# Kernel tuning notes

Hardware: AMD Instinct MI355X
Metric: run time of the kernel (lower is better)

## Reference

```python
import jax, jax.numpy as jnp
import numpy as np

B = 32          # graphs per batch
NPG = 2048      # nodes per graph
N = B * NPG     # 65536 total nodes
EPG = 16384     # edges per graph
E = B * EPG     # 524288 total edges
F_IN = 129
H, C = 4, 64    # heads, per-head channels
HC = H * C      # 256
NEG_SLOPE = 0.2 # GATConv LeakyReLU slope


def setup_inputs() -> dict:
    key = jax.random.key(0)
    ks = jax.random.split(key, 20)
    # node features
    x = jax.random.normal(ks[0], (N, F_IN), dtype=jnp.float32)
    # random edges, endpoints within the same graph (per-graph contiguous node ids)
    off = (jnp.arange(B) * NPG)[:, None]
    src = (jax.random.randint(ks[1], (B, EPG), 0, NPG) + off).reshape(-1)
    dst = (jax.random.randint(ks[2], (B, EPG), 0, NPG) + off).reshape(-1)
    edge_index = jnp.stack([src, dst]).astype(jnp.int64)

    def lin(k, fan_in, shape):
        return jax.random.normal(k, shape, dtype=jnp.float32) / np.sqrt(fan_in)

    return {
        "x": x,
        "edge_index": edge_index,
        "lin0_w": lin(ks[3], F_IN, (F_IN, 256)),
        "lin0_b": jnp.zeros((256,), jnp.float32),
        "gat0_W": lin(ks[4], 256, (256, HC)),
        "gat0_asrc": lin(ks[5], C, (H, C)),
        "gat0_adst": lin(ks[6], C, (H, C)),
        "gat0_b": jnp.zeros((HC,), jnp.float32),
        "pool0_w": lin(ks[7], HC, (HC,)),
        "gat1_W": lin(ks[8], HC, (HC, HC)),
        "gat1_asrc": lin(ks[9], C, (H, C)),
        "gat1_adst": lin(ks[10], C, (H, C)),
        "gat1_b": jnp.zeros((HC,), jnp.float32),
        "pool1_w": lin(ks[11], HC, (HC,)),
        "gate_w": lin(ks[12], HC, (HC, 1)),
        "gate_b": jnp.zeros((1,), jnp.float32),
    }


def _leaky(z):
    return jnp.where(z > 0, z, NEG_SLOPE * z)


def _gat(h_in, src, dst, emask, W, asrc, adst, b):
    """PyG GATConv: shared lin, edge attention, segment softmax over dest, self-loops, concat heads."""
    n = h_in.shape[0]
    h = (h_in @ W).reshape(n, H, C)                       # [n,H,C]
    loops = jnp.arange(n)
    s = jnp.concatenate([src, loops])                     # add self loops
    d = jnp.concatenate([dst, loops])
    m = jnp.concatenate([emask, jnp.ones((n,), bool)])
    a_s = jnp.einsum('nhc,hc->nh', h, asrc)               # [n,H]
    a_d = jnp.einsum('nhc,hc->nh', h, adst)
    logit = _leaky(a_s[s] + a_d[d])                       # [E+n,H]
    logit = jnp.where(m[:, None], logit, -1e9)
    mx = jax.ops.segment_max(logit, d, num_segments=n)    # stable segment softmax
    ex = jnp.exp(logit - mx[d]) * m[:, None].astype(logit.dtype)
    den = jax.ops.segment_sum(ex, d, num_segments=n)
    coef = ex / (den[d] + 1e-16)                          # [E+n,H]
    out = jax.ops.segment_sum(h[s] * coef[:, :, None], d, num_segments=n)
    return out.reshape(n, HC) + b


def _topk_pool(hx, src, dst, emask, w, n_in, k):
    """PyG TopKPooling: score = x.w/||w||, per-graph top-k, x' = x[perm]*tanh(score[perm]), edge filter+reindex."""
    n_tot = hx.shape[0]
    bb = n_tot // n_in
    score = (hx @ w) / (jnp.linalg.norm(w) + 1e-16)       # [n_tot]
    _, idx = jax.lax.top_k(score.reshape(bb, n_in), k)    # [bb,k]
    perm = (idx + (jnp.arange(bb) * n_in)[:, None]).reshape(-1)
    xs = hx[perm] * jnp.tanh(score[perm])[:, None]
    newid = jnp.full((n_tot,), -1, jnp.int32).at[perm].set(jnp.arange(bb * k, dtype=jnp.int32))
    ns, nd = newid[src], newid[dst]
    valid = emask & (ns >= 0) & (nd >= 0)
    ns = jnp.where(valid, ns, 0)
    nd = jnp.where(valid, nd, 0)
    return xs, ns, nd, valid


def _attpool(hx, n, gate_w, gate_b):
    """AttentionalAggregation: softmax(gate_nn(x)) per graph, weighted sum."""
    bb = hx.shape[0] // n
    gate = (hx @ gate_w + gate_b).reshape(bb, n)
    wts = jax.nn.softmax(gate, axis=1)
    return jnp.einsum('bn,bnf->bf', wts, hx.reshape(bb, n, -1))


def reference(x, edge_index, lin0_w, lin0_b, gat0_W, gat0_asrc, gat0_adst, gat0_b,
              pool0_w, gat1_W, gat1_asrc, gat1_adst, gat1_b, pool1_w, gate_w, gate_b):
    src, dst = edge_index[0], edge_index[1]
    emask = jnp.ones((E,), bool)
    h = jax.nn.relu(x @ lin0_w + lin0_b)                                  # hidden MLP
    h = jax.nn.elu(_gat(h, src, dst, emask, gat0_W, gat0_asrc, gat0_adst, gat0_b))
    h, src, dst, emask = _topk_pool(h, src, dst, emask, pool0_w, NPG, NPG // 2)
    out = _attpool(h, NPG // 2, gate_w, gate_b)                           # [B,256]
    h = jax.nn.elu(_gat(h, src, dst, emask, gat1_W, gat1_asrc, gat1_adst, gat1_b))
    h, src, dst, emask = _topk_pool(h, src, dst, emask, pool1_w, NPG // 2, NPG // 4)
    out = out + _attpool(h, NPG // 4, gate_w, gate_b)
    return out
```

## Files before the change

### kernel.cpp

```cpp
#include <hip/hip_runtime.h>
#include <cmath>

namespace {

constexpr int NN0 = 65536;
constexpr int NB  = 32;
constexpr int NE  = 524288;
constexpr int FIN = 129;
constexpr int KP  = 160;

typedef short bf16x8 __attribute__((ext_vector_type(8)));
typedef float f32x4 __attribute__((ext_vector_type(4)));

__device__ inline float leakyrelu(float z) { return z > 0.f ? z : 0.2f * z; }
__device__ inline float eluf(float z) { return z > 0.f ? z : expm1f(z); }

__device__ inline unsigned short f2bf(float x) {
  union { float f; unsigned int u; } v; v.f = x;
  unsigned int r = v.u + 0x7fffu + ((v.u >> 16) & 1u);
  return (unsigned short)(r >> 16);
}
__device__ inline float bf2f(unsigned short h) {
  union { unsigned int u; float f; } v; v.u = ((unsigned int)h) << 16;
  return v.f;
}

__device__ inline float4 f4fma(float4 a, float c, float4 acc) {
  acc.x += a.x * c; acc.y += a.y * c; acc.z += a.z * c; acc.w += a.w * c;
  return acc;
}

__device__ inline int swz_block(int bid, int bpgl) {
  int x = bid & 7;
  int local = bid >> 3;
  int g = x + ((local >> bpgl) << 3);
  return (g << bpgl) + (local & ((1 << bpgl) - 1));
}

__device__ __forceinline__ void gload_lds16(const unsigned short* g, unsigned short* l) {
  __builtin_amdgcn_global_load_lds((const unsigned int*)g, (unsigned int*)l, 16, 0, 0);
}

__device__ inline void pack_w_body(const float* __restrict__ W, int Kreal, int idx,
                                   unsigned short* __restrict__ hi,
                                   unsigned short* __restrict__ lo) {
  int j = idx & 7;
  int lane = (idx >> 3) & 63;
  int ct = (idx >> 9) & 15;
  int kt = idx >> 13;
  int k = kt * 32 + ((lane >> 4) << 3) + j;
  int c = ct * 16 + (lane & 15);
  float v = (k < Kreal) ? W[(size_t)k * 256 + c] : 0.f;
  unsigned short h = f2bf(v);
  hi[idx] = h;
  lo[idx] = f2bf(v - bf2f(h));
}

__global__ void prep(const float* __restrict__ x,
                     const float* __restrict__ w0, const float* __restrict__ w1,
                     const float* __restrict__ w2,
                     const float* __restrict__ pw0, const float* __restrict__ pw1,
                     unsigned short* __restrict__ xhi, unsigned short* __restrict__ xlo,
                     unsigned short* __restrict__ whi0, unsigned short* __restrict__ wlo0,
                     unsigned short* __restrict__ whi1, unsigned short* __restrict__ wlo1,
                     unsigned short* __restrict__ whi2, unsigned short* __restrict__ wlo2,
                     float* __restrict__ norms, int* __restrict__ cursor,
                     int* __restrict__ cursor2, int* __restrict__ newid) {
  const int NX = NN0 * KP / 256;
  const int NW0 = 5 * 8192 / 256;
  const int NW = 8 * 8192 / 256;
  const int NC = NN0 / 256;
  int b = blockIdx.x, tid = threadIdx.x;
  if (b < NX) {
    int idx = b * 256 + tid;
    int row = idx / KP, c = idx - row * KP;
    float v = (c < FIN) ? x[(size_t)row * FIN + c] : 0.f;
    unsigned short h = f2bf(v);
    xhi[idx] = h;
    xlo[idx] = f2bf(v - bf2f(h));
    return;
  }
  b -= NX;
  if (b < NW0) { pack_w_body(w0, FIN, b * 256 + tid, whi0, wlo0); return; }
  b -= NW0;
  if (b < NW) { pack_w_body(w1, 256, b * 256 + tid, whi1, wlo1); return; }
  b -= NW;
  if (b < NW) { pack_w_body(w2, 256, b * 256 + tid, whi2, wlo2); return; }
  b -= NW;
  if (b < NC) {
    int i = b * 256 + tid;
    cursor[i] = 0;
    newid[i] = -1;
    if (i < 32768) cursor2[i] = 0;
    return;
  }
  if (tid < 64) {
    float a0 = 0.f, a1 = 0.f;
#pragma unroll
    for (int j = tid; j < 256; j += 64) {
      float v0 = pw0[j]; a0 += v0 * v0;
      float v1 = pw1[j]; a1 += v1 * v1;
    }
#pragma unroll
    for (int off = 32; off >= 1; off >>= 1) {
      a0 += __shfl_xor(a0, off);
      a1 += __shfl_xor(a1, off);
    }
    if (tid == 0) {
      norms[0] = 1.f / (sqrtf(a0) + 1e-16f);
      norms[1] = 1.f / (sqrtf(a1) + 1e-16f);
    }
  }
}

template <int KT, bool RELUBIAS, bool ATT, bool INDIR>
__global__ __launch_bounds__(256, 2) void gemm_mfma(
    const unsigned short* __restrict__ Xhi, const unsigned short* __restrict__ Xlo,
    int ldx,
    const unsigned short* __restrict__ Bhi, const unsigned short* __restrict__ Blo,
    const float* __restrict__ bias,
    float* __restrict__ Out,
    unsigned short* __restrict__ OutHi, unsigned short* __restrict__ OutLo,
    const float* __restrict__ attsrc, const float* __restrict__ attdst,
    float* __restrict__ a_s, float* __restrict__ a_d,
    const int* __restrict__ rowmap, const float* __restrict__ tscale, int swzl) {
  __shared__ __align__(16) unsigned short As[2][2][128][32];
  const int tid = threadIdx.x;
  const int lane = tid & 63;
  const int w = tid >> 6;
  const int rb = (swzl >= 0) ? swz_block(blockIdx.x, swzl) : blockIdx.x;
  const int row0 = rb * 128;
  const int l15 = lane & 15, q = lane >> 4;
  const int sl4 = lane >> 2;
  const int skc = (lane & 3) * 8;

  size_t gr[2];
#pragma unroll
  for (int i = 0; i < 2; i++) {
    int lr = row0 + (w + 4 * i) * 16 + sl4;
    gr[i] = INDIR ? (size_t)rowmap[lr] : (size_t)lr;
  }

  auto stage = [&](int nb, int kt) {
#pragma unroll
    for (int i = 0; i < 2; i++) {
      const int rbase = (w + 4 * i) * 16;
      const size_t goff = gr[i] * ldx + kt * 32 + skc;
      gload_lds16(Xhi + goff, &As[nb][0][rbase][0]);
      gload_lds16(Xlo + goff, &As[nb][1][rbase][0]);
    }
  };

  f32x4 acc[8][4];
#pragma unroll
  for (int mf = 0; mf < 8; mf++)
#pragma unroll
    for (int nf = 0; nf < 4; nf++) acc[mf][nf] = (f32x4)(0.f);

  stage(0, 0);
  __syncthreads();

#pragma unroll
  for (int kt = 0; kt < KT; ++kt) {
    const int nb = kt & 1;
    if (kt + 1 < KT) stage(nb ^ 1, kt + 1);
    bf16x8 bh[4], bl[4];
#pragma unroll
    for (int nf = 0; nf < 4; nf++) {
      const int ct = w * 4 + nf;
      const size_t bbase = ((size_t)((kt * 16 + ct) * 64 + lane)) << 3;
      bh[nf] = *reinterpret_cast<const bf16x8*>(Bhi + bbase);
      bl[nf] = *reinterpret_cast<const bf16x8*>(Blo + bbase);
    }
#pragma unroll
    for (int mf = 0; mf < 8; mf++) {
      const int ar = mf * 16 + l15;
      bf16x8 ah = *reinterpret_cast<const bf16x8*>(&As[nb][0][ar][q * 8]);
      bf16x8 al = *reinterpret_cast<const bf16x8*>(&As[nb][1][ar][q * 8]);
#pragma unroll
      for (int nf = 0; nf < 4; nf++) {
        acc[mf][nf] = __builtin_amdgcn_mfma_f32_16x16x32_bf16(ah, bh[nf], acc[mf][nf], 0, 0, 0);
        acc[mf][nf] = __builtin_amdgcn_mfma_f32_16x16x32_bf16(ah, bl[nf], acc[mf][nf], 0, 0, 0);
        acc[mf][nf] = __builtin_amdgcn_mfma_f32_16x16x32_bf16(al, bh[nf], acc[mf][nf], 0, 0, 0);
      }
    }
    __syncthreads();
  }

#pragma unroll
  for (int mf = 0; mf < 8; mf++) {
    const int rowb = row0 + mf * 16 + q * 4;
#pragma unroll
    for (int r = 0; r < 4; r++) {
      const float ts = INDIR ? tscale[rowb + r] : 1.f;
#pragma unroll
      for (int nf = 0; nf < 4; nf++) {
        float v = acc[mf][nf][r];
        const int col = w * 64 + nf * 16 + l15;
        if constexpr (RELUBIAS) {
          v += bias[col];
          v = fmaxf(v, 0.f);
          unsigned short h = f2bf(v);
          OutHi[(size_t)(rowb + r) * 256 + col] = h;
          OutLo[(size_t)(rowb + r) * 256 + col] = f2bf(v - bf2f(h));
        } else {
          if constexpr (INDIR) v *= ts;
          Out[(size_t)(rowb + r) * 256 + col] = v;
        }
      }
    }
  }
  if constexpr (ATT) {
    const int head = w;
    float sv[4], dv[4];
#pragma unroll
    for (int nf = 0; nf < 4; nf++) {
      sv[nf] = attsrc[head * 64 + nf * 16 + l15];
      dv[nf] = attdst[head * 64 + nf * 16 + l15];
    }
#pragma unroll
    for (int mf = 0; mf < 8; mf++) {
#pragma unroll
      for (int r = 0; r < 4; r++) {
        float ps = 0.f, pd = 0.f;
#pragma unroll
        for (int nf = 0; nf < 4; nf++) {
          ps += acc[mf][nf][r] * sv[nf];
          pd += acc[mf][nf][r] * dv[nf];
        }
#pragma unroll
        for (int off = 8; off >= 1; off >>= 1) {
          ps += __shfl_xor(ps, off);
          pd += __shfl_xor(pd, off);
        }
        if (l15 == 0) {
          const int row = row0 + mf * 16 + q * 4 + r;
          float ts = INDIR ? tscale[row] : 1.f;
          a_s[(size_t)row * 4 + head] = ps * ts;
          a_d[(size_t)row * 4 + head] = pd * ts;
        }
      }
    }
  }
}

__global__ void scatter0(const int* __restrict__ src, const int* __restrict__ dst,
                         int* __restrict__ cursor, int* __restrict__ csr) {
  int e = blockIdx.x * blockDim.x + threadIdx.x;
  if (e >= NE) return;
  int d = dst[e];
  int pos = atomicAdd(&cursor[d], 1);
  if (pos < 64) csr[(size_t)d * 64 + pos] = src[e];
}

__global__ void scatter1(const int* __restrict__ src, const int* __restrict__ dst,
                         const int* __restrict__ newid,
                         int* __restrict__ cursor, int* __restrict__ csr) {
  int e = blockIdx.x * blockDim.x + threadIdx.x;
  if (e >= NE) return;
  int s = newid[src[e]], d = newid[dst[e]];
  if (s < 0 || d < 0) return;
  int pos = atomicAdd(&cursor[d], 1);
  if (pos < 64) csr[(size_t)d * 64 + pos] = s;
}

__global__ __launch_bounds__(256) void gat_node16(
    const int* __restrict__ cursor, const int* __restrict__ csr,
    const float* __restrict__ a_s, const float* __restrict__ a_d,
    const float* __restrict__ hW, const float* __restrict__ bias,
    const float* __restrict__ pool_w, const float* __restrict__ inv_norm,
    const float* __restrict__ gate_w,
    unsigned short* __restrict__ outHi, unsigned short* __restrict__ outLo,
    float* __restrict__ score, float* __restrict__ graw, int bpgl) {
  const int lane = threadIdx.x & 63;
  const int wv = threadIdx.x >> 6;
  const int dbase = swz_block(blockIdx.x, bpgl) * 16 + wv * 4;
  const int p = lane >> 4, l16 = lane & 15;

  const int d = dbase + p;
  const int deg = min(cursor[d], 63);
  const int dim = deg + 1;

  int dmaxw = dim;
  dmaxw = max(dmaxw, __shfl_xor(dmaxw, 16));
  dmaxw = max(dmaxw, __shfl_xor(dmaxw, 32));
  const int nch = (dmaxw + 15) >> 4;

  const float4 ad4 = *reinterpret_cast<const float4*>(&a_d[(size_t)d * 4]);

  int sreg[4];
  float L0[4], L1[4], L2[4], L3[4];
#pragma unroll
  for (int c = 0; c < 4; c++) {
    if (c < nch) {
      const int j = c * 16 + l16;
      const bool has = j < dim;
      int s = (j < deg) ? csr[(size_t)d * 64 + j] : d;
      sreg[c] = s;
      float4 as4 = *reinterpret_cast<const float4*>(&a_s[(size_t)s * 4]);
      L0[c] = has ? leakyrelu(as4.x + ad4.x) : -1e30f;
      L1[c] = has ? leakyrelu(as4.y + ad4.y) : -1e30f;
      L2[c] = has ? leakyrelu(as4.z + ad4.z) : -1e30f;
      L3[c] = has ? leakyrelu(as4.w + ad4.w) : -1e30f;
    } else {
      sreg[c] = d;
      L0[c] = -1e30f; L1[c] = -1e30f; L2[c] = -1e30f; L3[c] = -1e30f;
    }
  }
  float m0 = fmaxf(fmaxf(L0[0], L0[1]), fmaxf(L0[2], L0[3]));
  float m1 = fmaxf(fmaxf(L1[0], L1[1]), fmaxf(L1[2], L1[3]));
  float m2 = fmaxf(fmaxf(L2[0], L2[1]), fmaxf(L2[2], L2[3]));
  float m3 = fmaxf(fmaxf(L3[0], L3[1]), fmaxf(L3[2], L3[3]));
#pragma unroll
  for (int off = 1; off <= 8; off <<= 1) {
    m0 = fmaxf(m0, __shfl_xor(m0, off));
    m1 = fmaxf(m1, __shfl_xor(m1, off));
    m2 = fmaxf(m2, __shfl_xor(m2, off));
    m3 = fmaxf(m3, __shfl_xor(m3, off));
  }
  float e0[4], e1[4], e2[4], e3[4];
  float dn0 = 0.f, dn1 = 0.f, dn2 = 0.f, dn3 = 0.f;
#pragma unroll
  for (int c = 0; c < 4; c++) {
    if (c < nch) {
      e0[c] = __expf(L0[c] - m0);
      e1[c] = __expf(L1[c] - m1);
      e2[c] = __expf(L2[c] - m2);
      e3[c] = __expf(L3[c] - m3);
      dn0 += e0[c]; dn1 += e1[c]; dn2 += e2[c]; dn3 += e3[c];
    } else {
      e0[c] = 0.f; e1[c] = 0.f; e2[c] = 0.f; e3[c] = 0.f;
    }
  }
#pragma unroll
  for (int off = 1; off <= 8; off <<= 1) {
    dn0 += __shfl_xor(dn0, off);
    dn1 += __shfl_xor(dn1, off);
    dn2 += __shfl_xor(dn2, off);
    dn3 += __shfl_xor(dn3, off);
  }

  float4 acc[4];
#pragma unroll
  for (int h = 0; h < 4; h++) acc[h] = float4{0.f, 0.f, 0.f, 0.f};
#pragma unroll
  for (int c = 0; c < 4; c++) {
    if (c < nch) {
      const int tmax = min(16, dmaxw - c * 16);
#pragma unroll 2
      for (int tt = 0; tt < tmax; tt++) {
        const int idx = p * 16 + tt;
        int st = __shfl(sreg[c], idx);
        float c0 = __shfl(e0[c], idx), c1 = __shfl(e1[c], idx);
        float c2 = __shfl(e2[c], idx), c3 = __shfl(e3[c], idx);
        if (c * 16 + tt < dim) {
          const float4* hp = reinterpret_cast<const float4*>(&hW[(size_t)st * 256]) + l16;
          acc[0] = f4fma(hp[0],  c0, acc[0]);
          acc[1] = f4fma(hp[16], c1, acc[1]);
          acc[2] = f4fma(hp[32], c2, acc[2]);
          acc[3] = f4fma(hp[48], c3, acc[3]);
        }
      }
    }
  }

  const float inv[4] = {1.f / (dn0 + 1e-16f), 1.f / (dn1 + 1e-16f),
                        1.f / (dn2 + 1e-16f), 1.f / (dn3 + 1e-16f)};
  float sd = 0.f, gd = 0.f;
#pragma unroll
  for (int h = 0; h < 4; h++) {
    const int coff = h * 64 + l16 * 4;
    float4 bb = *reinterpret_cast<const float4*>(&bias[coff]);
    float4 o;
    o.x = eluf(acc[h].x * inv[h] + bb.x);
    o.y = eluf(acc[h].y * inv[h] + bb.y);
    o.z = eluf(acc[h].z * inv[h] + bb.z);
    o.w = eluf(acc[h].w * inv[h] + bb.w);
    ushort4 oh, ol;
    oh.x = f2bf(o.x); ol.x = f2bf(o.x - bf2f(oh.x));
    oh.y = f2bf(o.y); ol.y = f2bf(o.y - bf2f(oh.y));
    oh.z = f2bf(o.z); ol.z = f2bf(o.z - bf2f(oh.z));
    oh.w = f2bf(o.w); ol.w = f2bf(o.w - bf2f(oh.w));
    *reinterpret_cast<ushort4*>(&outHi[(size_t)d * 256 + coff]) = oh;
    *reinterpret_cast<ushort4*>(&outLo[(size_t)d * 256 + coff]) = ol;
    float4 pw = *reinterpret_cast<const float4*>(&pool_w[coff]);
    float4 gw = *reinterpret_cast<const float4*>(&gate_w[coff]);
    sd += o.x * pw.x + o.y * pw.y + o.z * pw.z + o.w * pw.w;
    gd += o.x * gw.x + o.y * gw.y + o.z * gw.z + o.w * gw.w;
  }
#pragma unroll
  for (int off = 1; off <= 8; off <<= 1) {
    sd += __shfl_xor(sd, off);
    gd += __shfl_xor(gd, off);
  }
  if (l16 == 0) {
    score[d] = sd * inv_norm[0];
    graw[d] = gd;
  }
}

__global__ __launch_bounds__(1024) void topk_hsel(
    const float* __restrict__ score, const float* __restrict__ graw,
    const float* __restrict__ gate_b, int npg, int k,
    int* __restrict__ perm, int* __restrict__ newid,
    float* __restrict__ gate, float* __restrict__ tsc) {
  __shared__ unsigned keys[2048];
  __shared__ int hist[1024];
  __shared__ int ssum[1024];
  __shared__ int segtot[16];
  __shared__ unsigned wmin[16], wmax[16];
  __shared__ int sstate[3];
  __shared__ int scnt;
  __shared__ int candi[512];
  __shared__ unsigned candk[512];
  const int g = blockIdx.x, tid = threadIdx.x;
  const int wv = tid >> 6, ln = tid & 63;
  const size_t base = (size_t)g * npg;

  unsigned mymin = 0xFFFFFFFFu, mymax = 0u;
  for (int i = tid; i < npg; i += 1024) {
    unsigned u = __float_as_uint(score[base + i]);
    u = (u & 0x80000000u) ? ~u : (u | 0x80000000u);
    keys[i] = u;
    mymin = min(mymin, u);
    mymax = max(mymax, u);
  }
#pragma unroll
  for (int off = 32; off >= 1; off >>= 1) {
    mymin = min(mymin, (unsigned)__shfl_xor((int)mymin, off));
    mymax = max(mymax, (unsigned)__shfl_xor((int)mymax, off));
  }
  if (ln == 0) { wmin[wv] = mymin; wmax[wv] = mymax; }
  __syncthreads();
  unsigned lo, hi;
  {
    unsigned a = 0xFFFFFFFFu, b = 0u;
#pragma unroll
    for (int i = 0; i < 16; i++) { a = min(a, wmin[i]); b = max(b, wmax[i]); }
    lo = a; hi = b;
  }
  int need = k;

  for (int iter = 0; iter < 4; ++iter) {
    unsigned long long range = (unsigned long long)(hi - lo) + 1ull;
    unsigned width = (unsigned)((range + 1023ull) >> 10);
    hist[tid] = 0;
    __syncthreads();
    for (int i = tid; i < npg; i += 1024) {
      unsigned u = keys[i];
      if (u >= lo && u <= hi) atomicAdd(&hist[(u - lo) / width], 1);
    }
    __syncthreads();
    int v = hist[tid];
    int s = v;
#pragma unroll
    for (int off = 1; off < 64; off <<= 1) {
      int t = __shfl_down(s, off);
      if (ln + off < 64) s += t;
    }
    if (ln == 0) segtot[wv] = s;
    __syncthreads();
    if (tid == 0) {
      int acc = 0;
      for (int i = 15; i >= 0; i--) { int t = segtot[i]; segtot[i] = acc; acc += t; }
    }
    __syncthreads();
    int S = s + segtot[wv];
    ssum[tid] = S;
    __syncthreads();
    int gt = (tid == 1023) ? 0 : ssum[tid + 1];
    if (S >= need && gt < need) {
      sstate[0] = tid;
      sstate[1] = gt;
      sstate[2] = hist[tid];
    }
    __syncthreads();
    const int bstar = sstate[0], cntAbove = sstate[1], m = sstate[2];
    unsigned nlo = lo + (unsigned)bstar * width;
    unsigned long long nhiu = (unsigned long long)lo + (unsigned long long)(bstar + 1) * width - 1ull;
    unsigned nhi = (nhiu > (unsigned long long)hi) ? hi : (unsigned)nhiu;
    need -= cntAbove;
    lo = nlo; hi = nhi;
    __syncthreads();
    if (width == 1 || m <= 256) break;
  }

  if (tid == 0) scnt = 0;
  __syncthreads();
  for (int i = tid; i < npg; i += 1024) {
    unsigned u = keys[i];
    if (u >= lo && u <= hi) {
      int pidx = atomicAdd(&scnt, 1);
      if (pidx < 512) { candi[pidx] = i; candk[pidx] = u; }
    }
  }
  __syncthreads();
  const int m_all = scnt;
  const float gb = gate_b[0];
  if (tid == 0) scnt = 0;
  __syncthreads();
  for (int i = tid; i < npg; i += 1024) {
    if (keys[i] > hi) {
      int pos = atomicAdd(&scnt, 1);
      int node = (int)(base + i);
      perm[g * k + pos] = node;
      if (newid) newid[node] = g * k + pos;
      float ts = tanhf(score[base + i]);
      tsc[g * k + pos] = ts;
      gate[g * k + pos] = ts * graw[node] + gb;
    }
  }
  __syncthreads();
  const int nAbove = scnt;
  if (m_all <= 512) {
    for (int c = tid; c < m_all; c += 1024) {
      unsigned u = candk[c];
      int i = candi[c];
      int rank = 0;
      for (int j = 0; j < m_all; j++) {
        unsigned vk = candk[j];
        rank += (vk > u) || (vk == u && candi[j] < i);
      }
      if (rank < need) {
        int pos = nAbove + rank;
        int node = (int)(base + i);
        perm[g * k + pos] = node;
        if (newid) newid[node] = g * k + pos;
        float ts = tanhf(score[base + i]);
        tsc[g * k + pos] = ts;
        gate[g * k + pos] = ts * graw[node] + gb;
      }
    }
  } else {
    for (int i = tid; i < npg; i += 1024) {
      unsigned u = keys[i];
      if (u >= lo && u <= hi) {
        int rank = 0;
        for (int j = 0; j < npg; j++) {
          unsigned vk = keys[j];
          if (vk >= lo && vk <= hi) rank += (vk > u) || (vk == u && j < i);
        }
        if (rank < need) {
          int pos = nAbove + rank;
          int node = (int)(base + i);
          perm[g * k + pos] = node;
          if (newid) newid[node] = g * k + pos;
          float ts = tanhf(score[base + i]);
          tsc[g * k + pos] = ts;
          gate[g * k + pos] = ts * graw[node] + gb;
        }
      }
    }
  }
}

__global__ __launch_bounds__(256) void attpool_sum(const unsigned short* __restrict__ xhi,
                                                   const unsigned short* __restrict__ xlo,
                                                   const int* __restrict__ perm,
                                                   const float* __restrict__ tsc,
                                                   const float* __restrict__ gate,
                                                   float* __restrict__ partials,
                                                   int npg, int bpgl) {
  int o = swz_block(blockIdx.x, bpgl);
  int g = o >> bpgl, sub = o & ((1 << bpgl) - 1);
  int tid = threadIdx.x;
  __shared__ float red[256];
  size_t base = (size_t)g * npg;
  float m = -1e30f;
  for (int i = tid; i < npg; i += 256) m = fmaxf(m, gate[base + i]);
  red[tid] = m;
  __syncthreads();
  for (int s = 128; s >= 1; s >>= 1) {
    if (tid < s) red[tid] = fmaxf(red[tid], red[tid + s]);
    __syncthreads();
  }
  m = red[0];
  __syncthreads();
  float ss = 0.f;
  for (int i = tid; i < npg; i += 256) ss += __expf(gate[base + i] - m);
  red[tid] = ss;
  __syncthreads();
  for (int s = 128; s >= 1; s >>= 1) {
    if (tid < s) red[tid] += red[tid + s];
    __syncthreads();
  }
  float inv = 1.f / red[0];
  __syncthreads();
  size_t r0 = base + sub * 32;
  int c = tid;
  float a = 0.f;
#pragma unroll 8
  for (int i = 0; i < 32; i++) {
    float wv = __expf(gate[r0 + i] - m) * inv * tsc[r0 + i];
    size_t node = (size_t)perm[r0 + i];
    float v = bf2f(xhi[node * 256 + c]) + bf2f(xlo[node * 256 + c]);
    a += wv * v;
  }
  partials[(size_t)o * 256 + c] = a;
}

__global__ __launch_bounds__(256) void attpool_reduce(const float* __restrict__ partials,
                                                      float* __restrict__ out,
                                                      int nch, int acc_flag) {
  int g = blockIdx.x, c = threadIdx.x;
  float a = 0.f;
  for (int s = 0; s < nch; s++) a += partials[((size_t)g * nch + s) * 256 + c];
  if (acc_flag) out[g * 256 + c] += a;
  else out[g * 256 + c] = a;
}

}

extern "C" void kernel_launch(void* const* d_in, const int* in_sizes, int n_in,
                              void* d_out, int out_size, void* d_ws, size_t ws_size,
                              hipStream_t stream) {
  (void)in_sizes; (void)n_in; (void)out_size; (void)ws_size;
  const float* x       = (const float*)d_in[0];
  const int*   ei      = (const int*)d_in[1];
  const float* lin0_w  = (const float*)d_in[2];
  const float* lin0_b  = (const float*)d_in[3];
  const float* gat0_W  = (const float*)d_in[4];
  const float* gat0_as = (const float*)d_in[5];
  const float* gat0_ad = (const float*)d_in[6];
  const float* gat0_b  = (const float*)d_in[7];
  const float* pool0_w = (const float*)d_in[8];
  const float* gat1_W  = (const float*)d_in[9];
  const float* gat1_as = (const float*)d_in[10];
  const float* gat1_ad = (const float*)d_in[11];
  const float* gat1_b  = (const float*)d_in[12];
  const float* pool1_w = (const float*)d_in[13];
  const float* gate_w  = (const float*)d_in[14];
  const float* gate_b  = (const float*)d_in[15];
  float* out = (float*)d_out;
  const int* srcp = ei;
  const int* dstp = ei + NE;

  char* wsb = (char*)d_ws;
  size_t cur = 0;
  auto alloc = [&](size_t bytes) {
    void* p = wsb + cur;
    cur = (cur + bytes + 255) & ~(size_t)255;
    return p;
  };
  char* regA = (char*)alloc((size_t)NN0 * 256 * 4);
  char* regB = (char*)alloc((size_t)NN0 * 256 * 4);
  char* regD = (char*)alloc((size_t)NN0 * KP * 2 * 2);
  float* a_s     = (float*)alloc((size_t)NN0 * 4 * 4);
  float* a_d     = (float*)alloc((size_t)NN0 * 4 * 4);
  int*   cursor  = (int*)alloc((size_t)NN0 * 4);
  int*   cursor2 = (int*)alloc((size_t)32768 * 4);
  int*   csr     = (int*)alloc((size_t)NN0 * 64 * 4);
  float* score   = (float*)alloc((size_t)NN0 * 4);
  float* graw    = (float*)alloc((size_t)NN0 * 4);
  int*   newid   = (int*)alloc((size_t)NN0 * 4);
  int*   perm0   = (int*)alloc((size_t)32768 * 4);
  int*   perm1   = (int*)alloc((size_t)16384 * 4);
  float* tsc0    = (float*)alloc((size_t)32768 * 4);
  float* tsc1    = (float*)alloc((size_t)16384 * 4);
  float* gate0   = (float*)alloc((size_t)32768 * 4);
  float* gate1   = (float*)alloc((size_t)16384 * 4);
  float* partials= (float*)alloc((size_t)NB * 32 * 256 * 4);
  float* norms   = (float*)alloc(2 * 4);
  unsigned short* whi0 = (unsigned short*)alloc((size_t)5 * 8192 * 2);
  unsigned short* wlo0 = (unsigned short*)alloc((size_t)5 * 8192 * 2);
  unsigned short* whi1 = (unsigned short*)alloc((size_t)8 * 8192 * 2);
  unsigned short* wlo1 = (unsigned short*)alloc((size_t)8 * 8192 * 2);
  unsigned short* whi2 = (unsigned short*)alloc((size_t)8 * 8192 * 2);
  unsigned short* wlo2 = (unsigned short*)alloc((size_t)8 * 8192 * 2);

  unsigned short* xhi = (unsigned short*)regD;
  unsigned short* xlo = xhi + (size_t)NN0 * KP;
  unsigned short* hhi = (unsigned short*)regA;
  unsigned short* hlo = hhi + (size_t)NN0 * 256;
  float* hW0  = (float*)regB;
  unsigned short* out0hi = (unsigned short*)regA;
  unsigned short* out0lo = out0hi + (size_t)NN0 * 256;
  float* hW1  = (float*)regB;
  unsigned short* out1hi = (unsigned short*)(regB + (size_t)32768 * 256 * 4);
  unsigned short* out1lo = out1hi + (size_t)32768 * 256;

  {
    int grid = NN0 * KP / 256 + 160 + 256 + 256 + 256 + 1;
    prep<<<grid, 256, 0, stream>>>(x, lin0_w, gat0_W, gat1_W, pool0_w, pool1_w,
                                   xhi, xlo, whi0, wlo0, whi1, wlo1, whi2, wlo2,
                                   norms, cursor, cursor2, newid);
  }

  gemm_mfma<5, true, false, false><<<NN0 / 128, 256, 0, stream>>>(
      xhi, xlo, KP, whi0, wlo0, lin0_b, nullptr, hhi, hlo,
      nullptr, nullptr, nullptr, nullptr, nullptr, nullptr, -1);

  scatter0<<<NE / 256, 256, 0, stream>>>(srcp, dstp, cursor, csr);
  gemm_mfma<8, false, true, false><<<NN0 / 128, 256, 0, stream>>>(
      hhi, hlo, 256, whi1, wlo1, nullptr, hW0, nullptr, nullptr,
      gat0_as, gat0_ad, a_s, a_d, nullptr, nullptr, -1);
  gat_node16<<<NN0 / 16, 256, 0, stream>>>(cursor, csr, a_s, a_d, hW0,
                                           gat0_b, pool0_w, norms, gate_w,
                                           out0hi, out0lo, score, graw, 7);

  topk_hsel<<<NB, 1024, 0, stream>>>(score, graw, gate_b, 2048, 1024,
                                     perm0, newid, gate0, tsc0);
  attpool_sum<<<NB * 32, 256, 0, stream>>>(out0hi, out0lo, perm0, tsc0, gate0,
                                           partials, 1024, 5);
  attpool_reduce<<<NB, 256, 0, stream>>>(partials, out, 32, 0);

  scatter1<<<NE / 256, 256, 0, stream>>>(srcp, dstp, newid, cursor2, csr);
  gemm_mfma<8, false, true, true><<<32768 / 128, 256, 0, stream>>>(
      out0hi, out0lo, 256, whi2, wlo2, nullptr, hW1, nullptr, nullptr,
      gat1_as, gat1_ad, a_s, a_d, perm0, tsc0, 3);
  gat_node16<<<32768 / 16, 256, 0, stream>>>(cursor2, csr, a_s, a_d, hW1,
                                             gat1_b, pool1_w, norms + 1, gate_w,
                                             out1hi, out1lo, score, graw, 6);

  topk_hsel<<<NB, 1024, 0, stream>>>(score, graw, gate_b, 1024, 512,
                                     perm1, nullptr, gate1, tsc1);
  attpool_sum<<<NB * 16, 256, 0, stream>>>(out1hi, out1lo, perm1, tsc1, gate1,
                                           partials, 512, 4);
  attpool_reduce<<<NB, 256, 0, stream>>>(partials, out, 16, 1);
}
```

Measured before the change: 303.1 us.

## Fuse lin0 and GAT0 GEMMs via LDS and use per-graph LDS-atomic CSR build

The input MLP GEMM and the first GAT linear GEMM now run in one kernel. The ReLU'd hidden activations are split into hi/lo bf16 and kept in swizzled shared memory, so the 65536x256 intermediate never goes through global memory. The edge scatter kernels now use one 1024-thread block per graph, counting with shared-memory atomics and writing the cursors at the end. That removes the global cursor zeroing and the global atomics. The tradeoffs are a smaller 64-row tile with about 72KB of LDS, which may limit occupancy, and only 32 blocks for the scatter, which leaves most CUs idle.

```diff
diff --git a/kernel.cpp b/kernel.cpp
--- a/kernel.cpp
+++ b/kernel.cpp
@@ -6,6 +6,7 @@
 constexpr int NN0 = 65536;
 constexpr int NB  = 32;
 constexpr int NE  = 524288;
+constexpr int EPG = 16384;
 constexpr int FIN = 129;
 constexpr int KP  = 160;
 
@@ -64,8 +65,7 @@
                      unsigned short* __restrict__ whi0, unsigned short* __restrict__ wlo0,
                      unsigned short* __restrict__ whi1, unsigned short* __restrict__ wlo1,
                      unsigned short* __restrict__ whi2, unsigned short* __restrict__ wlo2,
-                     float* __restrict__ norms, int* __restrict__ cursor,
-                     int* __restrict__ cursor2, int* __restrict__ newid) {
+                     float* __restrict__ norms, int* __restrict__ newid) {
   const int NX = NN0 * KP / 256;
   const int NW0 = 5 * 8192 / 256;
   const int NW = 8 * 8192 / 256;
@@ -88,10 +88,7 @@
   if (b < NW) { pack_w_body(w2, 256, b * 256 + tid, whi2, wlo2); return; }
   b -= NW;
   if (b < NC) {
-    int i = b * 256 + tid;
-    cursor[i] = 0;
-    newid[i] = -1;
-    if (i < 32768) cursor2[i] = 0;
+    newid[b * 256 + tid] = -1;
     return;
   }
   if (tid < 64) {
@@ -113,14 +110,161 @@
   }
 }
 
-template <int KT, bool RELUBIAS, bool ATT, bool INDIR>
+__global__ __launch_bounds__(256, 2) void gemm_fused(
+    const unsigned short* __restrict__ Xhi, const unsigned short* __restrict__ Xlo,
+    const unsigned short* __restrict__ B0hi, const unsigned short* __restrict__ B0lo,
+    const float* __restrict__ bias0,
+    const unsigned short* __restrict__ B1hi, const unsigned short* __restrict__ B1lo,
+    float* __restrict__ Out,
+    const float* __restrict__ attsrc, const float* __restrict__ attdst,
+    float* __restrict__ a_s, float* __restrict__ a_d) {
+  __shared__ __align__(16) unsigned short As[2][2][64][32];
+  __shared__ __align__(16) char Hsh[2][64 * 512];
+  const int tid = threadIdx.x;
+  const int lane = tid & 63;
+  const int w = tid >> 6;
+  const int row0 = blockIdx.x * 64;
+  const int l15 = lane & 15, q = lane >> 4;
+  const int srow16 = lane >> 2;
+  const int skc = (lane & 3) * 8;
+
+  auto stage = [&](int nb, int kt) {
+    const size_t goff = (size_t)(row0 + w * 16 + srow16) * KP + kt * 32 + skc;
+    gload_lds16(Xhi + goff, &As[nb][0][w * 16][0]);
+    gload_lds16(Xlo + goff, &As[nb][1][w * 16][0]);
+  };
+
+  f32x4 acc[4][4];
+#pragma unroll
+  for (int mf = 0; mf < 4; mf++)
+#pragma unroll
+    for (int nf = 0; nf < 4; nf++) acc[mf][nf] = (f32x4)(0.f);
+
+  stage(0, 0);
+  __syncthreads();
+
+#pragma unroll
+  for (int kt = 0; kt < 5; ++kt) {
+    const int nb = kt & 1;
+    if (kt + 1 < 5) stage(nb ^ 1, kt + 1);
+    bf16x8 bh[4], bl[4];
+#pragma unroll
+    for (int nf = 0; nf < 4; nf++) {
+      const int ct = w * 4 + nf;
+      const size_t bbase = ((size_t)((kt * 16 + ct) * 64 + lane)) << 3;
+      bh[nf] = *reinterpret_cast<const bf16x8*>(B0hi + bbase);
+      bl[nf] = *reinterpret_cast<const bf16x8*>(B0lo + bbase);
+    }
+#pragma unroll
+    for (int mf = 0; mf < 4; mf++) {
+      const int ar = mf * 16 + l15;
+      bf16x8 ah = *reinterpret_cast<const bf16x8*>(&As[nb][0][ar][q * 8]);
+      bf16x8 al = *reinterpret_cast<const bf16x8*>(&As[nb][1][ar][q * 8]);
+#pragma unroll
+      for (int nf = 0; nf < 4; nf++) {
+        acc[mf][nf] = __builtin_amdgcn_mfma_f32_16x16x32_bf16(ah, bh[nf], acc[mf][nf], 0, 0, 0);
+        acc[mf][nf] = __builtin_amdgcn_mfma_f32_16x16x32_bf16(ah, bl[nf], acc[mf][nf], 0, 0, 0);
+        acc[mf][nf] = __builtin_amdgcn_mfma_f32_16x16x32_bf16(al, bh[nf], acc[mf][nf], 0, 0, 0);
+      }
+    }
+    __syncthreads();
+  }
+
+#pragma unroll
+  for (int mf = 0; mf < 4; mf++) {
+#pragma unroll
+    for (int r = 0; r < 4; r++) {
+      const int row = mf * 16 + q * 4 + r;
+#pragma unroll
+      for (int nf = 0; nf < 4; nf++) {
+        const int col = w * 64 + nf * 16 + l15;
+        float v = acc[mf][nf][r] + bias0[col];
+        v = fmaxf(v, 0.f);
+        unsigned short h = f2bf(v);
+        unsigned short l = f2bf(v - bf2f(h));
+        unsigned int off = (unsigned int)(row * 512 + col * 2) ^ ((row & 7) << 4);
+        *reinterpret_cast<unsigned short*>(&Hsh[0][off]) = h;
+        *reinterpret_cast<unsigned short*>(&Hsh[1][off]) = l;
+        acc[mf][nf][r] = 0.f;
+      }
+    }
+  }
+  __syncthreads();
+
+#pragma unroll
+  for (int kt = 0; kt < 8; ++kt) {
+    bf16x8 bh[4], bl[4];
+#pragma unroll
+    for (int nf = 0; nf < 4; nf++) {
+      const int ct = w * 4 + nf;
+      const size_t bbase = ((size_t)((kt * 16 + ct) * 64 + lane)) << 3;
+      bh[nf] = *reinterpret_cast<const bf16x8*>(B1hi + bbase);
+      bl[nf] = *reinterpret_cast<const bf16x8*>(B1lo + bbase);
+    }
+#pragma unroll
+    for (int mf = 0; mf < 4; mf++) {
+      const int ar = mf * 16 + l15;
+      unsigned int off = (unsigned int)(ar * 512 + kt * 64 + q * 16) ^ ((ar & 7) << 4);
+      bf16x8 ah = *reinterpret_cast<const bf16x8*>(&Hsh[0][off]);
+      bf16x8 al = *reinterpret_cast<const bf16x8*>(&Hsh[1][off]);
+#pragma unroll
+      for (int nf = 0; nf < 4; nf++) {
+        acc[mf][nf] = __builtin_amdgcn_mfma_f32_16x16x32_bf16(ah, bh[nf], acc[mf][nf], 0, 0, 0);
+        acc[mf][nf] = __builtin_amdgcn_mfma_f32_16x16x32_bf16(ah, bl[nf], acc[mf][nf], 0, 0, 0);
+        acc[mf][nf] = __builtin_amdgcn_mfma_f32_16x16x32_bf16(al, bh[nf], acc[mf][nf], 0, 0, 0);
+      }
+    }
+  }
+
+#pragma unroll
+  for (int mf = 0; mf < 4; mf++) {
+    const int rowb = row0 + mf * 16 + q * 4;
+#pragma unroll
+    for (int r = 0; r < 4; r++) {
+#pragma unroll
+      for (int nf = 0; nf < 4; nf++) {
+        const int col = w * 64 + nf * 16 + l15;
+        Out[(size_t)(rowb + r) * 256 + col] = acc[mf][nf][r];
+      }
+    }
+  }
+  const int head = w;
+  float sv[4], dv[4];
+#pragma unroll
+  for (int nf = 0; nf < 4; nf++) {
+    sv[nf] = attsrc[head * 64 + nf * 16 + l15];
+    dv[nf] = attdst[head * 64 + nf * 16 + l15];
+  }
+#pragma unroll
+  for (int mf = 0; mf < 4; mf++) {
+#pragma unroll
+    for (int r = 0; r < 4; r++) {
+      float ps = 0.f, pd = 0.f;
+#pragma unroll
+      for (int nf = 0; nf < 4; nf++) {
+        ps += acc[mf][nf][r] * sv[nf];
+        pd += acc[mf][nf][r] * dv[nf];
+      }
+#pragma unroll
+      for (int off = 8; off >= 1; off >>= 1) {
+        ps += __shfl_xor(ps, off);
+        pd += __shfl_xor(pd, off);
+      }
+      if (l15 == 0) {
+        const int row = row0 + mf * 16 + q * 4 + r;
+        a_s[(size_t)row * 4 + head] = ps;
+        a_d[(size_t)row * 4 + head] = pd;
+      }
+    }
+  }
+}
+
+template <int KT, bool INDIR>
 __global__ __launch_bounds__(256, 2) void gemm_mfma(
     const unsigned short* __restrict__ Xhi, const unsigned short* __restrict__ Xlo,
     int ldx,
     const unsigned short* __restrict__ Bhi, const unsigned short* __restrict__ Blo,
-    const float* __restrict__ bias,
     float* __restrict__ Out,
-    unsigned short* __restrict__ OutHi, unsigned short* __restrict__ OutLo,
     const float* __restrict__ attsrc, const float* __restrict__ attdst,
     float* __restrict__ a_s, float* __restrict__ a_d,
     const int* __restrict__ rowmap, const float* __restrict__ tscale, int swzl) {
@@ -196,72 +340,84 @@
 #pragma unroll
       for (int nf = 0; nf < 4; nf++) {
         float v = acc[mf][nf][r];
+        if constexpr (INDIR) v *= ts;
         const int col = w * 64 + nf * 16 + l15;
-        if constexpr (RELUBIAS) {
-          v += bias[col];
-          v = fmaxf(v, 0.f);
-          unsigned short h = f2bf(v);
-          OutHi[(size_t)(rowb + r) * 256 + col] = h;
-          OutLo[(size_t)(rowb + r) * 256 + col] = f2bf(v - bf2f(h));
-        } else {
-          if constexpr (INDIR) v *= ts;
-          Out[(size_t)(rowb + r) * 256 + col] = v;
-        }
-      }
-    }
-  }
-  if constexpr (ATT) {
-    const int head = w;
-    float sv[4], dv[4];
-#pragma unroll
-    for (int nf = 0; nf < 4; nf++) {
-      sv[nf] = attsrc[head * 64 + nf * 16 + l15];
-      dv[nf] = attdst[head * 64 + nf * 16 + l15];
-    }
-#pragma unroll
-    for (int mf = 0; mf < 8; mf++) {
-#pragma unroll
-      for (int r = 0; r < 4; r++) {
-        float ps = 0.f, pd = 0.f;
-#pragma unroll
-        for (int nf = 0; nf < 4; nf++) {
-          ps += acc[mf][nf][r] * sv[nf];
-          pd += acc[mf][nf][r] * dv[nf];
-        }
-#pragma unroll
-        for (int off = 8; off >= 1; off >>= 1) {
-          ps += __shfl_xor(ps, off);
-          pd += __shfl_xor(pd, off);
-        }
-        if (l15 == 0) {
-          const int row = row0 + mf * 16 + q * 4 + r;
-          float ts = INDIR ? tscale[row] : 1.f;
-          a_s[(size_t)row * 4 + head] = ps * ts;
-          a_d[(size_t)row * 4 + head] = pd * ts;
-        }
-      }
-    }
-  }
-}
-
-__global__ void scatter0(const int* __restrict__ src, const int* __restrict__ dst,
-                         int* __restrict__ cursor, int* __restrict__ csr) {
-  int e = blockIdx.x * blockDim.x + threadIdx.x;
-  if (e >= NE) return;
-  int d = dst[e];
-  int pos = atomicAdd(&cursor[d], 1);
-  if (pos < 64) csr[(size_t)d * 64 + pos] = src[e];
-}
-
-__global__ void scatter1(const int* __restrict__ src, const int* __restrict__ dst,
-                         const int* __restrict__ newid,
-                         int* __restrict__ cursor, int* __restrict__ csr) {
-  int e = blockIdx.x * blockDim.x + threadIdx.x;
-  if (e >= NE) return;
-  int s = newid[src[e]], d = newid[dst[e]];
-  if (s < 0 || d < 0) return;
-  int pos = atomicAdd(&cursor[d], 1);
-  if (pos < 64) csr[(size_t)d * 64 + pos] = s;
+        Out[(size_t)(rowb + r) * 256 + col] = v;
+      }
+    }
+  }
+  const int head = w;
+  float sv[4], dv[4];
+#pragma unroll
+  for (int nf = 0; nf < 4; nf++) {
+    sv[nf] = attsrc[head * 64 + nf * 16 + l15];
+    dv[nf] = attdst[head * 64 + nf * 16 + l15];
+  }
+#pragma unroll
+  for (int mf = 0; mf < 8; mf++) {
+#pragma unroll
+    for (int r = 0; r < 4; r++) {
+      float ps = 0.f, pd = 0.f;
+#pragma unroll
+      for (int nf = 0; nf < 4; nf++) {
+        ps += acc[mf][nf][r] * sv[nf];
+        pd += acc[mf][nf][r] * dv[nf];
+      }
+#pragma unroll
+      for (int off = 8; off >= 1; off >>= 1) {
+        ps += __shfl_xor(ps, off);
+        pd += __shfl_xor(pd, off);
+      }
+      if (l15 == 0) {
+        const int row = row0 + mf * 16 + q * 4 + r;
+        float ts = INDIR ? tscale[row] : 1.f;
+        a_s[(size_t)row * 4 + head] = ps * ts;
+        a_d[(size_t)row * 4 + head] = pd * ts;
+      }
+    }
+  }
+}
+
+__global__ __launch_bounds__(1024) void scatter0L(const int* __restrict__ src,
+                                                  const int* __restrict__ dst,
+                                                  int* __restrict__ cursor,
+                                                  int* __restrict__ csr) {
+  __shared__ int cnt[2048];
+  const int g = blockIdx.x, tid = threadIdx.x;
+  cnt[tid] = 0;
+  cnt[tid + 1024] = 0;
+  __syncthreads();
+  const int e0 = g * EPG;
+  for (int i = tid; i < EPG; i += 1024) {
+    int e = e0 + i;
+    int d = dst[e];
+    int pos = atomicAdd(&cnt[d - (g << 11)], 1);
+    if (pos < 64) csr[(size_t)d * 64 + pos] = src[e];
+  }
+  __syncthreads();
+  cursor[(g << 11) + tid] = cnt[tid];
+  cursor[(g << 11) + tid + 1024] = cnt[tid + 1024];
+}
+
+__global__ __launch_bounds__(1024) void scatter1L(const int* __restrict__ src,
+                                                  const int* __restrict__ dst,
+                                                  const int* __restrict__ newid,
+                                                  int* __restrict__ cursor,
+                                                  int* __restrict__ csr) {
+  __shared__ int cnt[1024];
+  const int g = blockIdx.x, tid = threadIdx.x;
+  cnt[tid] = 0;
+  __syncthreads();
+  const int e0 = g * EPG;
+  for (int i = tid; i < EPG; i += 1024) {
+    int e = e0 + i;
+    int s = newid[src[e]], d = newid[dst[e]];
+    if (s < 0 || d < 0) continue;
+    int pos = atomicAdd(&cnt[d - (g << 10)], 1);
+    if (pos < 64) csr[(size_t)d * 64 + pos] = s;
+  }
+  __syncthreads();
+  cursor[(g << 10) + tid] = cnt[tid];
 }
 
 __global__ __launch_bounds__(256) void gat_node16(
@@ -670,8 +826,6 @@
 
   unsigned short* xhi = (unsigned short*)regD;
   unsigned short* xlo = xhi + (size_t)NN0 * KP;
-  unsigned short* hhi = (unsigned short*)regA;
-  unsigned short* hlo = hhi + (size_t)NN0 * 256;
   float* hW0  = (float*)regB;
   unsigned short* out0hi = (unsigned short*)regA;
   unsigned short* out0lo = out0hi + (size_t)NN0 * 256;
@@ -683,17 +837,15 @@
     int grid = NN0 * KP / 256 + 160 + 256 + 256 + 256 + 1;
     prep<<<grid, 256, 0, stream>>>(x, lin0_w, gat0_W, gat1_W, pool0_w, pool1_w,
                                    xhi, xlo, whi0, wlo0, whi1, wlo1, whi2, wlo2,
-                                   norms, cursor, cursor2, newid);
-  }
-
-  gemm_mfma<5, true, false, false><<<NN0 / 128, 256, 0, stream>>>(
-      xhi, xlo, KP, whi0, wlo0, lin0_b, nullptr, hhi, hlo,
-      nullptr, nullptr, nullptr, nullptr, nullptr, nullptr, -1);
-
-  scatter0<<<NE / 256, 256, 0, stream>>>(srcp, dstp, cursor, csr);
-  gemm_mfma<8, false, true, false><<<NN0 / 128, 256, 0, stream>>>(
-      hhi, hlo, 256, whi1, wlo1, nullptr, hW0, nullptr, nullptr,
-      gat0_as, gat0_ad, a_s, a_d, nullptr, nullptr, -1);
+                                   norms, newid);
+  }
+
+  scatter0L<<<NB, 1024, 0, stream>>>(srcp, dstp, cursor, csr);
+
+  gemm_fused<<<NN0 / 64, 256, 0, stream>>>(
+      xhi, xlo, whi0, wlo0, lin0_b, whi1, wlo1, hW0,
+      gat0_as, gat0_ad, a_s, a_d);
+
   gat_node16<<<NN0 / 16, 256, 0, stream>>>(cursor, csr, a_s, a_d, hW0,
                                            gat0_b, pool0_w, norms, gate_w,
                                            out0hi, out0lo, score, graw, 7);
@@ -704,9 +856,9 @@
                                            partials, 1024, 5);
   attpool_reduce<<<NB, 256, 0, stream>>>(partials, out, 32, 0);
 
-  scatter1<<<NE / 256, 256, 0, stream>>>(srcp, dstp, newid, cursor2, csr);
-  gemm_mfma<8, false, true, true><<<32768 / 128, 256, 0, stream>>>(
-      out0hi, out0lo, 256, whi2, wlo2, nullptr, hW1, nullptr, nullptr,
+  scatter1L<<<NB, 1024, 0, stream>>>(srcp, dstp, newid, cursor2, csr);
+  gemm_mfma<8, true><<<32768 / 128, 256, 0, stream>>>(
+      out0hi, out0lo, 256, whi2, wlo2, hW1,
       gat1_as, gat1_ad, a_s, a_d, perm0, tsc0, 3);
   gat_node16<<<32768 / 16, 256, 0, stream>>>(cursor2, csr, a_s, a_d, hW1,
                                              gat1_b, pool1_w, norms + 1, gate_w,
```

New measurement: 280.7 us. 1.08x faster.
